# Kernel optimization log

Hardware: AMD Instinct MI355X
Metric: run time of the kernel (lower is better)

The kernel has to match this reference:

```python
import jax, jax.numpy as jnp
import numpy as np
from jax import lax

B, L, N = 64, 1024, 64
IN_SZ, MEM_SZ, DEC = 128, 1024, 3


def setup_inputs() -> dict:
    key = jax.random.key(0)
    ks = jax.random.split(key, 8)
    x = jax.random.normal(ks[0], (B, L, N), dtype=jnp.float32)
    # sensor net: Linear(N -> IN_SZ) with bias (stored as [in, out])
    W_sense = jax.random.normal(ks[1], (N, IN_SZ), dtype=jnp.float32) / np.sqrt(N)
    b_sense = jax.random.normal(ks[2], (IN_SZ,), dtype=jnp.float32) * 0.01
    # nBRC: ff_im Linear(IN_SZ -> 3*MEM_SZ, bias=False), ff_mm Linear(MEM_SZ -> 2*MEM_SZ, bias=False)
    W_im = jax.random.normal(ks[3], (IN_SZ, 3 * MEM_SZ), dtype=jnp.float32) / np.sqrt(IN_SZ)
    W_mm = jax.random.normal(ks[4], (MEM_SZ, 2 * MEM_SZ), dtype=jnp.float32) / np.sqrt(MEM_SZ)
    # actor net: Linear(MEM_SZ -> DEC) with bias
    W_act = jax.random.normal(ks[5], (MEM_SZ, DEC), dtype=jnp.float32) / np.sqrt(MEM_SZ)
    b_act = jax.random.normal(ks[6], (DEC,), dtype=jnp.float32) * 0.01
    return {"x": x, "W_sense": W_sense, "b_sense": b_sense,
            "W_im": W_im, "W_mm": W_mm, "W_act": W_act, "b_act": b_act}


def reference(x, W_sense, b_sense, W_im, W_mm, W_act, b_act):
    # sense: applied per-token (flattened in torch; equivalent broadcasted matmul)
    inputs = x @ W_sense + b_sense                      # [B, L, IN_SZ]
    # precompute the input projection for all timesteps in one GEMM
    proj = inputs @ W_im                                 # [B, L, 3*MEM_SZ]
    proj_t = jnp.moveaxis(proj, 1, 0)                    # [L, B, 3*MEM_SZ]
    h0 = jnp.zeros((x.shape[0], MEM_SZ), dtype=x.dtype)

    def step(h, p):
        i_a, i_c, i_o = jnp.split(p, 3, axis=-1)         # each [B, MEM_SZ]
        m = h @ W_mm                                      # [B, 2*MEM_SZ]
        m_a, m_c = jnp.split(m, 2, axis=-1)
        a = 1.0 + jnp.tanh(i_a + m_a)
        c = jax.nn.sigmoid(i_c + m_c)
        hn = c * h + (1.0 - c) * jnp.tanh(i_o + a * h)
        return hn, hn

    _, hs = lax.scan(step, h0, proj_t)                    # [L, B, MEM_SZ]
    memory = jnp.moveaxis(hs, 0, 1)                       # [B, L, MEM_SZ]
    logits = memory @ W_act + b_act                       # [B, L, DEC]
    return jax.nn.softmax(logits, axis=-1)
```

## Files before the change

### kernel.cpp

```cpp
#include <hip/hip_runtime.h>
#include <hip/hip_bf16.h>


#define B_TOT 64
#define L_SEQ 1024
#define N_IN 64
#define INSZ 128
#define MEM 1024
#define DEC 3

#define NGROUP 8
#define BG 8
#define NMEM 32
#define RING 16

typedef __hip_bfloat16 bf16;
typedef short bf16x8 __attribute__((ext_vector_type(8)));
typedef float f32x4 __attribute__((ext_vector_type(4)));
typedef int i32x4 __attribute__((ext_vector_type(4)));
typedef unsigned long long ull;

#define OFF_INPUTS 0
#define SZ_INPUTS  (L_SEQ * 64 * INSZ * 2)
#define OFF_WMM    (OFF_INPUTS + SZ_INPUTS)
#define SZ_WMM     (128 * 32 * 64 * 8 * 2)
#define OFF_WIM    (OFF_WMM + SZ_WMM)
#define SZ_WIM     (192 * 4 * 64 * 8 * 2)
#define OFF_HBUF   (OFF_WIM + SZ_WIM)
#define SZ_HBUF    (RING * NGROUP * BG * MEM * 2)
#define OFF_CTR    (OFF_HBUF + SZ_HBUF)
#define SZ_CTR     ((8192 + 256) * 4)

__device__ __forceinline__ float fast_tanh(float x) {
    float e = __expf(2.f * x);
    return 1.f - 2.f / (e + 1.f);
}
__device__ __forceinline__ float fast_sigmoid(float x) {
    return 1.f / (1.f + __expf(-x));
}

__global__ void k_sense(const float* __restrict__ x, const float* __restrict__ Ws,
                        const float* __restrict__ bs, bf16* __restrict__ inputs) {
    int t = blockIdx.x;
    int tid = threadIdx.x;
    __shared__ float xls[64][64];
    __shared__ float wls[64][128];
    for (int idx = tid; idx < 64 * 64; idx += 256) {
        int b = idx >> 6, k = idx & 63;
        xls[b][k] = x[((size_t)b * L_SEQ + t) * N_IN + k];
    }
    for (int idx = tid; idx < 64 * 128; idx += 256) {
        int k = idx >> 7, j = idx & 127;
        wls[k][j] = Ws[k * INSZ + j];
    }
    __syncthreads();
    int j = tid & 127;
    int bh = tid >> 7;
    float bj = bs[j];
    for (int bi = 0; bi < 32; ++bi) {
        int b = bh * 32 + bi;
        float acc = bj;
#pragma unroll
        for (int k = 0; k < 64; ++k) acc += xls[b][k] * wls[k][j];
        inputs[((size_t)t * 64 + b) * INSZ + j] = (bf16)acc;
    }
}

__global__ void k_pack(const float* __restrict__ Wmm, const float* __restrict__ Wim,
                       bf16* __restrict__ pmm, bf16* __restrict__ pim) {
    int idx = blockIdx.x * 256 + threadIdx.x;
    const int NMMF = 128 * 32 * 64 * 8;
    if (idx < NMMF) {
        int j = idx & 7, lane = (idx >> 3) & 63, kb = (idx >> 9) & 31, ct = idx >> 14;
        int n = ct * 16 + (lane & 15);
        int k = kb * 32 + ((lane >> 4) << 3) + j;
        pmm[idx] = (bf16)Wmm[(size_t)k * 2048 + n];
    } else {
        int idx2 = idx - NMMF;
        if (idx2 < 192 * 4 * 64 * 8) {
            int j = idx2 & 7, lane = (idx2 >> 3) & 63, kb = (idx2 >> 9) & 3, ct = idx2 >> 11;
            int n = ct * 16 + (lane & 15);
            int k = kb * 32 + ((lane >> 4) << 3) + j;
            pim[idx2] = (bf16)Wim[(size_t)k * 3072 + n];
        }
    }
}

__launch_bounds__(256, 1)
__global__ void k_main(const bf16* __restrict__ inputs, const bf16* __restrict__ pmm,
                       const bf16* __restrict__ pim, const float* __restrict__ Wact,
                       const float* __restrict__ bact, bf16* __restrict__ hbuf,
                       float* __restrict__ out, unsigned int* __restrict__ ctr) {
    const int g = blockIdx.x & 7;
    const int m = blockIdx.x >> 3;
    const int tid = (int)threadIdx.x;
    const int wave = tid >> 6;
    const int lane = tid & 63;
    const int r16 = lane & 15;
    const int q = lane >> 4;
    const int col = tid & 31;
    const int p = col >> 4;
    const int cl = col & 15;
    const int bloc = tid >> 5;

    __shared__ float ilds[2][3][2][8][16];
    __shared__ float mpart[4][4][8][16];
    __shared__ bf16 hstage[8][32];
    __shared__ float wact_lds[3072];
    __shared__ float aplds[4][3];
    __shared__ float bactl[3];
    __shared__ unsigned idsl[256];
    __shared__ int fflagl;
    __shared__ float outbuf[L_SEQ * 3];

    for (int idx = tid; idx < 3072; idx += 256) wact_lds[idx] = Wact[idx];
    if (tid < 3) bactl[tid] = bact[tid];

    bf16x8 wb[4][8];
    {
        int base_ct[4] = {2 * m, 2 * m + 1, 64 + 2 * m, 65 + 2 * m};
#pragma unroll
        for (int t4 = 0; t4 < 4; ++t4)
#pragma unroll
            for (int kk = 0; kk < 8; ++kk)
                wb[t4][kk] = *(const bf16x8*)(pmm +
                    (((size_t)base_ct[t4] * 32 + (wave * 8 + kk)) * 64 + lane) * 8);
    }
    bf16x8 wi[2][4];
    if (wave < 3) {
#pragma unroll
        for (int tl = 0; tl < 2; ++tl) {
            int ct2 = wave * 64 + m * 2 + tl;
#pragma unroll
            for (int kb2 = 0; kb2 < 4; ++kb2)
                wi[tl][kb2] = *(const bf16x8*)(pim + (((size_t)ct2 * 4 + kb2) * 64 + lane) * 8);
        }
    }
    float hreg = 0.f;

    unsigned int* flags   = ctr + g * 512;
    unsigned int* flagsL2 = ctr + 4096 + g * 512;
    unsigned int* ids     = ctr + 8192;

    unsigned xid;
    asm volatile("s_getreg_b32 %0, hwreg(HW_REG_XCC_ID)" : "=s"(xid));
    if (tid == 0)
        __hip_atomic_store(&ids[g * 32 + m], xid + 1u, __ATOMIC_RELAXED,
                           __HIP_MEMORY_SCOPE_AGENT);
    if (wave == 0) {
        int sb = 1 << 20;
        unsigned v0 = 0, v1 = 0, v2 = 0, v3 = 0;
        bool all = false;
        while (!all && --sb > 0) {
            v0 = __hip_atomic_load(&ids[lane], __ATOMIC_RELAXED, __HIP_MEMORY_SCOPE_AGENT);
            v1 = __hip_atomic_load(&ids[64 + lane], __ATOMIC_RELAXED, __HIP_MEMORY_SCOPE_AGENT);
            v2 = __hip_atomic_load(&ids[128 + lane], __ATOMIC_RELAXED, __HIP_MEMORY_SCOPE_AGENT);
            v3 = __hip_atomic_load(&ids[192 + lane], __ATOMIC_RELAXED, __HIP_MEMORY_SCOPE_AGENT);
            all = (bool)__all((int)(v0 && v1 && v2 && v3));
        }
        idsl[lane] = v0; idsl[64 + lane] = v1; idsl[128 + lane] = v2; idsl[192 + lane] = v3;
    }
    __syncthreads();
    if (tid == 0) {
        int f = 1;
        for (int g2 = 0; g2 < 8; ++g2) {
            unsigned r = idsl[g2 * 32];
            for (int k2 = 1; k2 < 32; ++k2) f &= (idsl[g2 * 32 + k2] == r);
        }
        fflagl = f;
    }
    __syncthreads();
    const bool fastf = (fflagl != 0);

    struct I2 { f32x4 a0, a1; };
    auto comp_iacc = [&](int t) -> I2 {
        I2 r;
        r.a0 = (f32x4){0.f, 0.f, 0.f, 0.f};
        r.a1 = (f32x4){0.f, 0.f, 0.f, 0.f};
        if (wave < 3) {
            int brow = g * 8 + (r16 & 7);
#pragma unroll
            for (int kb2 = 0; kb2 < 4; ++kb2) {
                bf16x8 af = *(const bf16x8*)(inputs +
                    ((size_t)t * 64 + brow) * INSZ + kb2 * 32 + q * 8);
                r.a0 = __builtin_amdgcn_mfma_f32_16x16x32_bf16(af, wi[0][kb2], r.a0, 0, 0, 0);
                r.a1 = __builtin_amdgcn_mfma_f32_16x16x32_bf16(af, wi[1][kb2], r.a1, 0, 0, 0);
            }
        }
        return r;
    };

    auto poll_own = [&](unsigned target) {
        int k = wave * 8 + (lane & 7);
        bool act = lane < 8;
        unsigned vbest = act ? 0u : target;
        bool done = false;
        int rounds = 0;
        int sb = 1 << 20;
        while (!done && --sb > 0) {
            if (fastf && act && vbest < target) {
                const unsigned* a = flagsL2 + k * 16;
                unsigned vl;
                asm volatile("global_load_dword %0, %1, off sc0\n\t"
                             "s_waitcnt vmcnt(0)"
                             : "=&v"(vl) : "v"(a) : "memory");
                if (vl > vbest) vbest = vl;
            }
            if (act && vbest < target && (!fastf || rounds >= 2)) {
                unsigned vm = __hip_atomic_load(&flags[k * 16], __ATOMIC_RELAXED,
                                                __HIP_MEMORY_SCOPE_AGENT);
                if (vm > vbest) vbest = vm;
            }
            done = (bool)__all((int)(vbest >= target));
            ++rounds;
            if (!done && rounds > 8) __builtin_amdgcn_s_sleep(1);
        }
    };

    auto actor_emit = [&](int t_src) {
        int c0 = tid * 4;
        const bf16* hp = hbuf +
            ((size_t)(((t_src & (RING - 1)) * NGROUP + g)) * (BG * MEM)) +
            (c0 >> 5) * 256 + m * 32 + (c0 & 31);
        ushort4 hv = *(const ushort4*)hp;
        float h0 = __uint_as_float((unsigned)hv.x << 16);
        float h1 = __uint_as_float((unsigned)hv.y << 16);
        float h2 = __uint_as_float((unsigned)hv.z << 16);
        float h3 = __uint_as_float((unsigned)hv.w << 16);
        const f32x4* wp = (const f32x4*)&wact_lds[c0 * 3];
        f32x4 w0 = wp[0], w1 = wp[1], w2 = wp[2];
        float p0 = h0 * w0[0] + h1 * w0[3] + h2 * w1[2] + h3 * w2[1];
        float p1 = h0 * w0[1] + h1 * w1[0] + h2 * w1[3] + h3 * w2[2];
        float p2 = h0 * w0[2] + h1 * w1[1] + h2 * w2[0] + h3 * w2[3];
#pragma unroll
        for (int off = 32; off >= 1; off >>= 1) {
            p0 += __shfl_xor(p0, off);
            p1 += __shfl_xor(p1, off);
            p2 += __shfl_xor(p2, off);
        }
        if (lane == 0) { aplds[wave][0] = p0; aplds[wave][1] = p1; aplds[wave][2] = p2; }
    };
    auto actor_fin = [&](int tout) {
        float l0 = aplds[0][0] + aplds[1][0] + aplds[2][0] + aplds[3][0] + bactl[0];
        float l1 = aplds[0][1] + aplds[1][1] + aplds[2][1] + aplds[3][1] + bactl[1];
        float l2 = aplds[0][2] + aplds[1][2] + aplds[2][2] + aplds[3][2] + bactl[2];
        float mx = fmaxf(l0, fmaxf(l1, l2));
        float e0 = __expf(l0 - mx), e1 = __expf(l1 - mx), e2 = __expf(l2 - mx);
        float inv = 1.f / (e0 + e1 + e2);
        outbuf[tout * 3 + 0] = e0 * inv;
        outbuf[tout * 3 + 1] = e1 * inv;
        outbuf[tout * 3 + 2] = e2 * inv;
    };

    I2 iacc = comp_iacc(0);

#pragma clang loop unroll(disable)
    for (int t = 0; t < L_SEQ; ++t) {
        if (t != 0 && (t & (RING - 1)) == 0)
            __builtin_amdgcn_fence(__ATOMIC_ACQUIRE, "agent");

        if (wave < 3 && q < 2) {
#pragma unroll
            for (int reg = 0; reg < 4; ++reg) {
                ilds[t & 1][wave][0][q * 4 + reg][r16] = iacc.a0[reg];
                ilds[t & 1][wave][1][q * 4 + reg][r16] = iacc.a1[reg];
            }
        }

        if (t > 0) poll_own((unsigned)t);

        {
            const bf16* lp = hbuf +
                ((size_t)((((t - 1) & (RING - 1)) * NGROUP + g)) * (BG * MEM)) +
                (size_t)(wave * 8) * 256 + ((r16 & 7) * 32 + q * 8);
            bf16x8 af[8];
#pragma unroll
            for (int kk = 0; kk < 8; ++kk)
                af[kk] = *(const bf16x8*)(lp + kk * 256);
            f32x4 acc0 = {0.f, 0.f, 0.f, 0.f};
            f32x4 acc1 = {0.f, 0.f, 0.f, 0.f};
            f32x4 acc2 = {0.f, 0.f, 0.f, 0.f};
            f32x4 acc3 = {0.f, 0.f, 0.f, 0.f};
#pragma unroll
            for (int kk = 0; kk < 8; ++kk) {
                acc0 = __builtin_amdgcn_mfma_f32_16x16x32_bf16(af[kk], wb[0][kk], acc0, 0, 0, 0);
                acc1 = __builtin_amdgcn_mfma_f32_16x16x32_bf16(af[kk], wb[1][kk], acc1, 0, 0, 0);
                acc2 = __builtin_amdgcn_mfma_f32_16x16x32_bf16(af[kk], wb[2][kk], acc2, 0, 0, 0);
                acc3 = __builtin_amdgcn_mfma_f32_16x16x32_bf16(af[kk], wb[3][kk], acc3, 0, 0, 0);
            }
            if (q < 2) {
#pragma unroll
                for (int reg = 0; reg < 4; ++reg) {
                    mpart[wave][0][q * 4 + reg][r16] = acc0[reg];
                    mpart[wave][1][q * 4 + reg][r16] = acc1[reg];
                    mpart[wave][2][q * 4 + reg][r16] = acc2[reg];
                    mpart[wave][3][q * 4 + reg][r16] = acc3[reg];
                }
            }
        }
        __syncthreads();

        if (m < 8 && t >= 2 && tid == 64) actor_fin(t - 2);

        {
            float ma = mpart[0][p][bloc][cl] + mpart[1][p][bloc][cl]
                     + mpart[2][p][bloc][cl] + mpart[3][p][bloc][cl];
            float mc = mpart[0][2 + p][bloc][cl] + mpart[1][2 + p][bloc][cl]
                     + mpart[2][2 + p][bloc][cl] + mpart[3][2 + p][bloc][cl];
            float ia = ilds[t & 1][0][p][bloc][cl];
            float ic = ilds[t & 1][1][p][bloc][cl];
            float io = ilds[t & 1][2][p][bloc][cl];
            float a = 1.f + fast_tanh(ia + ma);
            float c = fast_sigmoid(ic + mc);
            float hn = c * hreg + (1.f - c) * fast_tanh(io + a * hreg);
            hreg = hn;
            hstage[bloc][col] = (bf16)hn;
        }
        __syncthreads();

        if (wave == 3) {
            bf16* base = hbuf +
                ((size_t)(((t & (RING - 1)) * NGROUP + g)) * (BG * MEM)) + m * 256;
            int row = lane >> 3, c = lane & 7;
            ull v = *(const ull*)(&hstage[row][c * 4]);
            ull* dst = (ull*)base + lane;
            if (fastf) {
                *dst = v;
            } else {
                __hip_atomic_store(dst, v, __ATOMIC_RELAXED, __HIP_MEMORY_SCOPE_AGENT);
            }
            asm volatile("s_waitcnt vmcnt(0)" ::: "memory");
            if (lane == 0) {
                if (fastf) flagsL2[m * 16] = (unsigned)(t + 1);
                __hip_atomic_store(&flags[m * 16], (unsigned)(t + 1), __ATOMIC_RELAXED,
                                   __HIP_MEMORY_SCOPE_AGENT);
            }
        }
        if (t + 1 < L_SEQ) iacc = comp_iacc(t + 1);
        if (m < 8 && t > 0) actor_emit(t - 1);
    }

    if (m < 8) {
        __syncthreads();
        if (tid == 0) actor_fin(L_SEQ - 2);
        poll_own((unsigned)L_SEQ);
        __builtin_amdgcn_fence(__ATOMIC_ACQUIRE, "agent");
        __syncthreads();
        actor_emit(L_SEQ - 1);
        __syncthreads();
        if (tid == 0) actor_fin(L_SEQ - 1);
        __syncthreads();
        float* obase = out + (size_t)(g * 8 + m) * L_SEQ * 3;
        for (int idx = tid; idx < L_SEQ * 3; idx += 256)
            obase[idx] = outbuf[idx];
    }
}

extern "C" void kernel_launch(void* const* d_in, const int* in_sizes, int n_in,
                              void* d_out, int out_size, void* d_ws, size_t ws_size,
                              hipStream_t stream) {
    const float* x    = (const float*)d_in[0];
    const float* Ws   = (const float*)d_in[1];
    const float* bs   = (const float*)d_in[2];
    const float* Wim  = (const float*)d_in[3];
    const float* Wmm  = (const float*)d_in[4];
    const float* Wact = (const float*)d_in[5];
    const float* bact = (const float*)d_in[6];

    char* ws = (char*)d_ws;
    bf16* inputs = (bf16*)(ws + OFF_INPUTS);
    bf16* pmm    = (bf16*)(ws + OFF_WMM);
    bf16* pim    = (bf16*)(ws + OFF_WIM);
    bf16* hbuf   = (bf16*)(ws + OFF_HBUF);
    unsigned int* ctr = (unsigned int*)(ws + OFF_CTR);

    hipMemsetAsync(hbuf, 0, SZ_HBUF, stream);
    hipMemsetAsync(ctr, 0, SZ_CTR, stream);

    k_sense<<<L_SEQ, 256, 0, stream>>>(x, Ws, bs, inputs);
    k_pack<<<(128 * 32 * 64 * 8 + 192 * 4 * 64 * 8) / 256, 256, 0, stream>>>(Wmm, Wim, pmm, pim);
    k_main<<<NGROUP * NMEM, 256, 0, stream>>>(inputs, pmm, pim, Wact, bact, hbuf,
                                              (float*)d_out, ctr);
}
```

Baseline: 3.322 ms.

## Move gate update and publish onto one wave, drop per-step barrier

The elementwise gate update and h publish now run on wave 3 alone, each lane handling four elements read vectorised from double-buffered LDS partials. This removes the second __syncthreads per timestep and the hstage staging round-trip. Meanwhile waves 0-2 compute the next step's input projection (inputs loaded one step earlier) and the actor logits for the previous step. mpart and aplds are double-buffered to make this safe. The cost is a serial elementwise phase on one wave, plus more register and LDS pressure.

```diff
diff --git a/kernel.cpp b/kernel.cpp
--- a/kernel.cpp
+++ b/kernel.cpp
@@ -98,16 +98,11 @@
     const int lane = tid & 63;
     const int r16 = lane & 15;
     const int q = lane >> 4;
-    const int col = tid & 31;
-    const int p = col >> 4;
-    const int cl = col & 15;
-    const int bloc = tid >> 5;
 
     __shared__ float ilds[2][3][2][8][16];
-    __shared__ float mpart[4][4][8][16];
-    __shared__ bf16 hstage[8][32];
+    __shared__ float mpart[2][4][4][8][16];
     __shared__ float wact_lds[3072];
-    __shared__ float aplds[4][3];
+    __shared__ float aplds[2][4][3];
     __shared__ float bactl[3];
     __shared__ unsigned idsl[256];
     __shared__ int fflagl;
@@ -136,7 +131,12 @@
                 wi[tl][kb2] = *(const bf16x8*)(pim + (((size_t)ct2 * 4 + kb2) * 64 + lane) * 8);
         }
     }
-    float hreg = 0.f;
+
+    f32x4 hreg = {0.f, 0.f, 0.f, 0.f};
+    const int erow = lane >> 3;
+    const int ec = lane & 7;
+    const int ep = ec >> 2;
+    const int ecl = (ec & 3) * 4;
 
     unsigned int* flags   = ctr + g * 512;
     unsigned int* flagsL2 = ctr + 4096 + g * 512;
@@ -172,22 +172,33 @@
     __syncthreads();
     const bool fastf = (fflagl != 0);
 
-    struct I2 { f32x4 a0, a1; };
-    auto comp_iacc = [&](int t) -> I2 {
-        I2 r;
-        r.a0 = (f32x4){0.f, 0.f, 0.f, 0.f};
-        r.a1 = (f32x4){0.f, 0.f, 0.f, 0.f};
+    bf16x8 afin[4];
+    auto load_in = [&](int t) {
         if (wave < 3) {
             int brow = g * 8 + (r16 & 7);
+            const bf16* src = inputs + ((size_t)t * 64 + brow) * INSZ + q * 8;
+#pragma unroll
+            for (int kb2 = 0; kb2 < 4; ++kb2)
+                afin[kb2] = *(const bf16x8*)(src + kb2 * 32);
+        }
+    };
+    auto mma_in_deposit = [&](int t) {
+        if (wave < 3) {
+            f32x4 a0 = (f32x4){0.f, 0.f, 0.f, 0.f};
+            f32x4 a1 = (f32x4){0.f, 0.f, 0.f, 0.f};
 #pragma unroll
             for (int kb2 = 0; kb2 < 4; ++kb2) {
-                bf16x8 af = *(const bf16x8*)(inputs +
-                    ((size_t)t * 64 + brow) * INSZ + kb2 * 32 + q * 8);
-                r.a0 = __builtin_amdgcn_mfma_f32_16x16x32_bf16(af, wi[0][kb2], r.a0, 0, 0, 0);
-                r.a1 = __builtin_amdgcn_mfma_f32_16x16x32_bf16(af, wi[1][kb2], r.a1, 0, 0, 0);
-            }
-        }
-        return r;
+                a0 = __builtin_amdgcn_mfma_f32_16x16x32_bf16(afin[kb2], wi[0][kb2], a0, 0, 0, 0);
+                a1 = __builtin_amdgcn_mfma_f32_16x16x32_bf16(afin[kb2], wi[1][kb2], a1, 0, 0, 0);
+            }
+            if (q < 2) {
+#pragma unroll
+                for (int reg = 0; reg < 4; ++reg) {
+                    ilds[t & 1][wave][0][q * 4 + reg][r16] = a0[reg];
+                    ilds[t & 1][wave][1][q * 4 + reg][r16] = a1[reg];
+                }
+            }
+        }
     };
 
     auto poll_own = [&](unsigned target) {
@@ -217,33 +228,43 @@
         }
     };
 
-    auto actor_emit = [&](int t_src) {
-        int c0 = tid * 4;
+    auto hload = [&](int t_src, int gg) -> ushort4 {
+        int c0 = gg * 4;
         const bf16* hp = hbuf +
             ((size_t)(((t_src & (RING - 1)) * NGROUP + g)) * (BG * MEM)) +
             (c0 >> 5) * 256 + m * 32 + (c0 & 31);
-        ushort4 hv = *(const ushort4*)hp;
+        return *(const ushort4*)hp;
+    };
+    auto emit_accum = [&](ushort4 hv, int gg, float& p0, float& p1, float& p2) {
+        int c0 = gg * 4;
         float h0 = __uint_as_float((unsigned)hv.x << 16);
         float h1 = __uint_as_float((unsigned)hv.y << 16);
         float h2 = __uint_as_float((unsigned)hv.z << 16);
         float h3 = __uint_as_float((unsigned)hv.w << 16);
         const f32x4* wp = (const f32x4*)&wact_lds[c0 * 3];
         f32x4 w0 = wp[0], w1 = wp[1], w2 = wp[2];
-        float p0 = h0 * w0[0] + h1 * w0[3] + h2 * w1[2] + h3 * w2[1];
-        float p1 = h0 * w0[1] + h1 * w1[0] + h2 * w1[3] + h3 * w2[2];
-        float p2 = h0 * w0[2] + h1 * w1[1] + h2 * w2[0] + h3 * w2[3];
+        p0 += h0 * w0[0] + h1 * w0[3] + h2 * w1[2] + h3 * w2[1];
+        p1 += h0 * w0[1] + h1 * w1[0] + h2 * w1[3] + h3 * w2[2];
+        p2 += h0 * w0[2] + h1 * w1[1] + h2 * w2[0] + h3 * w2[3];
+    };
+    auto emit_reduce = [&](int t_src, float p0, float p1, float p2) {
 #pragma unroll
         for (int off = 32; off >= 1; off >>= 1) {
             p0 += __shfl_xor(p0, off);
             p1 += __shfl_xor(p1, off);
             p2 += __shfl_xor(p2, off);
         }
-        if (lane == 0) { aplds[wave][0] = p0; aplds[wave][1] = p1; aplds[wave][2] = p2; }
-    };
-    auto actor_fin = [&](int tout) {
-        float l0 = aplds[0][0] + aplds[1][0] + aplds[2][0] + aplds[3][0] + bactl[0];
-        float l1 = aplds[0][1] + aplds[1][1] + aplds[2][1] + aplds[3][1] + bactl[1];
-        float l2 = aplds[0][2] + aplds[1][2] + aplds[2][2] + aplds[3][2] + bactl[2];
+        if (lane == 0) {
+            aplds[t_src & 1][wave][0] = p0;
+            aplds[t_src & 1][wave][1] = p1;
+            aplds[t_src & 1][wave][2] = p2;
+        }
+    };
+    auto fin = [&](int tout) {
+        int pr = tout & 1;
+        float l0 = aplds[pr][0][0] + aplds[pr][1][0] + aplds[pr][2][0] + bactl[0];
+        float l1 = aplds[pr][0][1] + aplds[pr][1][1] + aplds[pr][2][1] + bactl[1];
+        float l2 = aplds[pr][0][2] + aplds[pr][1][2] + aplds[pr][2][2] + bactl[2];
         float mx = fmaxf(l0, fmaxf(l1, l2));
         float e0 = __expf(l0 - mx), e1 = __expf(l1 - mx), e2 = __expf(l2 - mx);
         float inv = 1.f / (e0 + e1 + e2);
@@ -252,20 +273,52 @@
         outbuf[tout * 3 + 2] = e2 * inv;
     };
 
-    I2 iacc = comp_iacc(0);
+    auto ew_publish = [&](int t) {
+        int par = t & 1;
+        f32x4 ma = *(const f32x4*)&mpart[par][0][ep][erow][ecl];
+        f32x4 mc = *(const f32x4*)&mpart[par][0][2 + ep][erow][ecl];
+#pragma unroll
+        for (int w = 1; w < 4; ++w) {
+            ma += *(const f32x4*)&mpart[par][w][ep][erow][ecl];
+            mc += *(const f32x4*)&mpart[par][w][2 + ep][erow][ecl];
+        }
+        f32x4 ia = *(const f32x4*)&ilds[par][0][ep][erow][ecl];
+        f32x4 ic = *(const f32x4*)&ilds[par][1][ep][erow][ecl];
+        f32x4 io = *(const f32x4*)&ilds[par][2][ep][erow][ecl];
+        bf16 hb[4];
+#pragma unroll
+        for (int i = 0; i < 4; ++i) {
+            float a = 1.f + fast_tanh(ia[i] + ma[i]);
+            float c = fast_sigmoid(ic[i] + mc[i]);
+            float hn = c * hreg[i] + (1.f - c) * fast_tanh(io[i] + a * hreg[i]);
+            hreg[i] = hn;
+            hb[i] = (bf16)hn;
+        }
+        ull v = *(const ull*)hb;
+        bf16* base = hbuf +
+            ((size_t)(((t & (RING - 1)) * NGROUP + g)) * (BG * MEM)) + m * 256;
+        ull* dst = (ull*)base + lane;
+        if (fastf) {
+            *dst = v;
+        } else {
+            __hip_atomic_store(dst, v, __ATOMIC_RELAXED, __HIP_MEMORY_SCOPE_AGENT);
+        }
+        asm volatile("s_waitcnt vmcnt(0)" ::: "memory");
+        if (lane == 0) {
+            if (fastf) flagsL2[m * 16] = (unsigned)(t + 1);
+            __hip_atomic_store(&flags[m * 16], (unsigned)(t + 1), __ATOMIC_RELAXED,
+                               __HIP_MEMORY_SCOPE_AGENT);
+        }
+    };
+
+    load_in(0);
+    mma_in_deposit(0);
+    load_in(1);
 
 #pragma clang loop unroll(disable)
     for (int t = 0; t < L_SEQ; ++t) {
         if (t != 0 && (t & (RING - 1)) == 0)
             __builtin_amdgcn_fence(__ATOMIC_ACQUIRE, "agent");
-
-        if (wave < 3 && q < 2) {
-#pragma unroll
-            for (int reg = 0; reg < 4; ++reg) {
-                ilds[t & 1][wave][0][q * 4 + reg][r16] = iacc.a0[reg];
-                ilds[t & 1][wave][1][q * 4 + reg][r16] = iacc.a1[reg];
-            }
-        }
 
         if (t > 0) poll_own((unsigned)t);
 
@@ -291,64 +344,54 @@
             if (q < 2) {
 #pragma unroll
                 for (int reg = 0; reg < 4; ++reg) {
-                    mpart[wave][0][q * 4 + reg][r16] = acc0[reg];
-                    mpart[wave][1][q * 4 + reg][r16] = acc1[reg];
-                    mpart[wave][2][q * 4 + reg][r16] = acc2[reg];
-                    mpart[wave][3][q * 4 + reg][r16] = acc3[reg];
+                    mpart[t & 1][wave][0][q * 4 + reg][r16] = acc0[reg];
+                    mpart[t & 1][wave][1][q * 4 + reg][r16] = acc1[reg];
+                    mpart[t & 1][wave][2][q * 4 + reg][r16] = acc2[reg];
+                    mpart[t & 1][wave][3][q * 4 + reg][r16] = acc3[reg];
                 }
             }
         }
+        ushort4 eh0;
+        if (m < 8 && t > 0 && wave < 3) eh0 = hload(t - 1, tid);
         __syncthreads();
 
-        if (m < 8 && t >= 2 && tid == 64) actor_fin(t - 2);
-
-        {
-            float ma = mpart[0][p][bloc][cl] + mpart[1][p][bloc][cl]
-                     + mpart[2][p][bloc][cl] + mpart[3][p][bloc][cl];
-            float mc = mpart[0][2 + p][bloc][cl] + mpart[1][2 + p][bloc][cl]
-                     + mpart[2][2 + p][bloc][cl] + mpart[3][2 + p][bloc][cl];
-            float ia = ilds[t & 1][0][p][bloc][cl];
-            float ic = ilds[t & 1][1][p][bloc][cl];
-            float io = ilds[t & 1][2][p][bloc][cl];
-            float a = 1.f + fast_tanh(ia + ma);
-            float c = fast_sigmoid(ic + mc);
-            float hn = c * hreg + (1.f - c) * fast_tanh(io + a * hreg);
-            hreg = hn;
-            hstage[bloc][col] = (bf16)hn;
-        }
-        __syncthreads();
-
         if (wave == 3) {
-            bf16* base = hbuf +
-                ((size_t)(((t & (RING - 1)) * NGROUP + g)) * (BG * MEM)) + m * 256;
-            int row = lane >> 3, c = lane & 7;
-            ull v = *(const ull*)(&hstage[row][c * 4]);
-            ull* dst = (ull*)base + lane;
-            if (fastf) {
-                *dst = v;
-            } else {
-                __hip_atomic_store(dst, v, __ATOMIC_RELAXED, __HIP_MEMORY_SCOPE_AGENT);
-            }
-            asm volatile("s_waitcnt vmcnt(0)" ::: "memory");
-            if (lane == 0) {
-                if (fastf) flagsL2[m * 16] = (unsigned)(t + 1);
-                __hip_atomic_store(&flags[m * 16], (unsigned)(t + 1), __ATOMIC_RELAXED,
-                                   __HIP_MEMORY_SCOPE_AGENT);
-            }
-        }
-        if (t + 1 < L_SEQ) iacc = comp_iacc(t + 1);
-        if (m < 8 && t > 0) actor_emit(t - 1);
+            ew_publish(t);
+        } else {
+            ushort4 eh1;
+            if (m < 8 && t > 0 && wave == 0) eh1 = hload(t - 1, tid + 192);
+            if (t + 1 < L_SEQ) mma_in_deposit(t + 1);
+            if (t + 2 < L_SEQ) load_in(t + 2);
+            if (m < 8) {
+                if (t >= 2 && tid == 64) fin(t - 2);
+                if (t > 0) {
+                    float p0 = 0.f, p1 = 0.f, p2 = 0.f;
+                    emit_accum(eh0, tid, p0, p1, p2);
+                    if (wave == 0) emit_accum(eh1, tid + 192, p0, p1, p2);
+                    emit_reduce(t - 1, p0, p1, p2);
+                }
+            }
+        }
     }
 
     if (m < 8) {
         __syncthreads();
-        if (tid == 0) actor_fin(L_SEQ - 2);
+        if (tid == 64) fin(L_SEQ - 2);
         poll_own((unsigned)L_SEQ);
         __builtin_amdgcn_fence(__ATOMIC_ACQUIRE, "agent");
         __syncthreads();
-        actor_emit(L_SEQ - 1);
+        if (wave < 3) {
+            float p0 = 0.f, p1 = 0.f, p2 = 0.f;
+            ushort4 a = hload(L_SEQ - 1, tid);
+            emit_accum(a, tid, p0, p1, p2);
+            if (wave == 0) {
+                ushort4 b = hload(L_SEQ - 1, tid + 192);
+                emit_accum(b, tid + 192, p0, p1, p2);
+            }
+            emit_reduce(L_SEQ - 1, p0, p1, p2);
+        }
         __syncthreads();
-        if (tid == 0) actor_fin(L_SEQ - 1);
+        if (tid == 0) fin(L_SEQ - 1);
         __syncthreads();
         float* obase = out + (size_t)(g * 8 + m) * L_SEQ * 3;
         for (int idx = tid; idx < L_SEQ * 3; idx += 256)
```

Measured after the change: 3.051 ms. 1.09x faster.
